# Kernel optimization log

Measured on AMD Instinct MI355X. Metric: run time of the kernel, lower is better.

Reference implementation:

```python
import jax, jax.numpy as jnp
import numpy as np

V = 1_000_000
D = 128
HS = 128
NUM_GRAPHS = 16384  # static segment count (== batch.max()+1 in the torch code)


def setup_inputs() -> dict:
    key = jax.random.key(0)
    k1, k2, k3, k4, k5 = jax.random.split(key, 5)
    H = jax.random.normal(k1, (V, D), dtype=jnp.float32)
    batch = jnp.sort(jax.random.randint(k2, (V,), 0, NUM_GRAPHS, dtype=jnp.int64))
    # nn.Linear-style init scale
    W_proj = jax.random.normal(k3, (HS, D), dtype=jnp.float32) * (1.0 / np.sqrt(D))
    b_proj = jax.random.normal(k4, (HS,), dtype=jnp.float32) * (1.0 / np.sqrt(D))
    w_score = jax.random.normal(k5, (HS,), dtype=jnp.float32) * (1.0 / np.sqrt(HS))
    return {"H": H, "batch": batch, "W_proj": W_proj, "b_proj": b_proj, "w_score": w_score}


def reference(H, batch, W_proj, b_proj, w_score):
    # e_v = a^T tanh(W h_v)            -> [V]
    e = jnp.tanh(H @ W_proj.T + b_proj) @ w_score
    # per-graph segment softmax (stable: shift by segment max)
    max_per_g = jax.ops.segment_max(e, batch, num_segments=NUM_GRAPHS)  # [G]
    a = jnp.exp(e - max_per_g[batch])
    denom = jax.ops.segment_sum(a, batch, num_segments=NUM_GRAPHS)  # [G]
    alpha = a / jnp.maximum(denom[batch], 1e-12)
    # weighted sum pooling: h_G = sum_v alpha_v h_v  -> [G, D]
    out = jax.ops.segment_sum(alpha[:, None] * H, batch, num_segments=NUM_GRAPHS)
    return out
```

## Files before the change

### kernel.cpp

```cpp
#include <hip/hip_runtime.h>
#include <hip/hip_bf16.h>
#include <hip/hip_fp16.h>

typedef __bf16 bf16x8 __attribute__((ext_vector_type(8)));
typedef float f32x4 __attribute__((ext_vector_type(4)));

constexpr int NUM_G = 16384;
constexpr int DIM = 128;
constexpr int CHUNK = 64;
constexpr int GRID1 = 768;

__global__ void seg_starts_kernel(const int* __restrict__ batch, int* __restrict__ seg, int V) {
    int v = blockIdx.x * blockDim.x + threadIdx.x;
    if (v >= V) return;
    int b1 = batch[v];
    int b0 = (v == 0) ? -1 : batch[v - 1];
    for (int g = b0 + 1; g <= b1; ++g) seg[g] = v;
    if (v == V - 1)
        for (int g = b1 + 1; g <= NUM_G; ++g) seg[g] = V;
}

__launch_bounds__(256, 3)
__global__ void attn_agg_kernel(const float* __restrict__ Hm,
                                const float* __restrict__ Wp,
                                const float* __restrict__ bp,
                                const float* __restrict__ wsc,
                                const int* __restrict__ seg,
                                float* __restrict__ out) {
    __shared__ __align__(16) __bf16 Hs[CHUNK * DIM];
    __shared__ float e_part[2][CHUNK];
    __shared__ float alpha_s[CHUNK];
    __shared__ float red[4];

    const int t = threadIdx.x;
    const int lane = t & 63;
    const int wave = t >> 6;
    const int l15 = lane & 15;
    const int lq = lane >> 4;
    const int mgrp = wave >> 1;
    const int nhalf = wave & 1;

    bf16x8 bfrag[4][4];
    float bias_n[4], wsc_n[4];
#pragma unroll
    for (int nt = 0; nt < 4; ++nt) {
        int n_g = (nhalf * 4 + nt) * 16 + l15;
        bias_n[nt] = bp[n_g];
        wsc_n[nt] = wsc[n_g];
#pragma unroll
        for (int ks = 0; ks < 4; ++ks) {
            const float* src = Wp + n_g * DIM + ks * 32 + lq * 8;
            f32x4 w0 = *(const f32x4*)src;
            f32x4 w1 = *(const f32x4*)(src + 4);
            bf16x8 f;
            f[0] = (__bf16)w0[0]; f[1] = (__bf16)w0[1]; f[2] = (__bf16)w0[2]; f[3] = (__bf16)w0[3];
            f[4] = (__bf16)w1[0]; f[5] = (__bf16)w1[1]; f[6] = (__bf16)w1[2]; f[7] = (__bf16)w1[3];
            bfrag[nt][ks] = f;
        }
    }

    for (int g = blockIdx.x; g < NUM_G; g += GRID1) {
        int v0 = seg[g];
        int n = seg[g + 1] - v0;
        float acc = 0.f;
        float lsum = 0.f;

        for (int r0 = 0; r0 < n; r0 += CHUNK) {
            int c = min(CHUNK, n - r0);
            __syncthreads();

            for (int i = t; i < c * 16; i += 256) {
                int row = i >> 4, ch = i & 15;
                const float* src = Hm + (size_t)(v0 + r0 + row) * DIM + ch * 8;
                f32x4 a0 = *(const f32x4*)src;
                f32x4 a1 = *(const f32x4*)(src + 4);
                bf16x8 hv;
                hv[0] = (__bf16)a0[0]; hv[1] = (__bf16)a0[1]; hv[2] = (__bf16)a0[2]; hv[3] = (__bf16)a0[3];
                hv[4] = (__bf16)a1[0]; hv[5] = (__bf16)a1[1]; hv[6] = (__bf16)a1[2]; hv[7] = (__bf16)a1[3];
                int chs = ch ^ (row & 15);
                *(bf16x8*)&Hs[row * DIM + chs * 8] = hv;
            }
            __syncthreads();

#pragma unroll
            for (int mt = 0; mt < 2; ++mt) {
                int mtile = mgrp * 2 + mt;
                int arow = mtile * 16 + l15;
                bf16x8 afrag[4];
#pragma unroll
                for (int ks = 0; ks < 4; ++ks) {
                    int chs = (ks * 4 + lq) ^ l15;
                    afrag[ks] = *(const bf16x8*)&Hs[arow * DIM + chs * 8];
                }
                float epl[4] = {0.f, 0.f, 0.f, 0.f};
#pragma unroll
                for (int nt = 0; nt < 4; ++nt) {
                    f32x4 dacc = {0.f, 0.f, 0.f, 0.f};
#pragma unroll
                    for (int ks = 0; ks < 4; ++ks)
                        dacc = __builtin_amdgcn_mfma_f32_16x16x32_bf16(afrag[ks], bfrag[nt][ks], dacc, 0, 0, 0);
#pragma unroll
                    for (int r = 0; r < 4; ++r) {
                        float x = dacc[r] + bias_n[nt];
                        float ex = __expf(2.f * x);
                        float th = 1.f - 2.f * __builtin_amdgcn_rcpf(ex + 1.f);
                        epl[r] += th * wsc_n[nt];
                    }
                }
#pragma unroll
                for (int m = 1; m < 16; m <<= 1)
#pragma unroll
                    for (int r = 0; r < 4; ++r)
                        epl[r] += __shfl_xor(epl[r], m, 64);
                if (l15 == 0)
#pragma unroll
                    for (int r = 0; r < 4; ++r)
                        e_part[nhalf][mtile * 16 + lq * 4 + r] = epl[r];
            }
            __syncthreads();

            float pv = 0.f;
            if (t < c) {
                float ev = e_part[0][t] + e_part[1][t];
                float p = __expf(ev);
                alpha_s[t] = p;
                pv = p;
            }
#pragma unroll
            for (int m = 1; m < 64; m <<= 1) pv += __shfl_xor(pv, m, 64);
            if (lane == 0) red[wave] = pv;
            __syncthreads();
            lsum += red[0] + red[1] + red[2] + red[3];

            if (t < 128) {
                int dch = t >> 3, doff = t & 7;
                int r = 0;
                for (; r + 4 <= c; r += 4) {
                    float p0 = alpha_s[r],     p1 = alpha_s[r + 1];
                    float p2 = alpha_s[r + 2], p3 = alpha_s[r + 3];
                    float h0 = (float)Hs[(r)     * DIM + ((dch ^ ((r)     & 15)) * 8) + doff];
                    float h1 = (float)Hs[(r + 1) * DIM + ((dch ^ ((r + 1) & 15)) * 8) + doff];
                    float h2 = (float)Hs[(r + 2) * DIM + ((dch ^ ((r + 2) & 15)) * 8) + doff];
                    float h3 = (float)Hs[(r + 3) * DIM + ((dch ^ ((r + 3) & 15)) * 8) + doff];
                    acc += p0 * h0 + p1 * h1 + p2 * h2 + p3 * h3;
                }
                for (; r < c; ++r)
                    acc += alpha_s[r] * (float)Hs[r * DIM + ((dch ^ (r & 15)) * 8) + doff];
            }
        }

        if (t < 128)
            out[(size_t)g * DIM + t] = acc / fmaxf(lsum, 1e-12f);
    }
}

extern "C" void kernel_launch(void* const* d_in, const int* in_sizes, int n_in,
                              void* d_out, int out_size, void* d_ws, size_t ws_size,
                              hipStream_t stream) {
    const float* Hm  = (const float*)d_in[0];
    const int* batch = (const int*)d_in[1];
    const float* Wp  = (const float*)d_in[2];
    const float* bp  = (const float*)d_in[3];
    const float* wsc = (const float*)d_in[4];
    float* out = (float*)d_out;
    int* seg = (int*)d_ws;
    int V = in_sizes[1];

    seg_starts_kernel<<<(V + 255) / 256, 256, 0, stream>>>(batch, seg, V);
    attn_agg_kernel<<<GRID1, 256, 0, stream>>>(Hm, Wp, bp, wsc, seg, out);
}
```

Measured before the change: 722.6 us.

## Launch one block per graph, double chunk size, split pooling across all threads

Replaces the persistent grid-stride loop over graphs with one block per graph (16384 blocks). The chunk grows from 64 to 128 rows, with MFMA tiles guarded by row count. The weighted-sum pooling now uses all 256 threads, each half taking alternate rows, and the halves are combined through shared memory at the end. The aim is better load balance and more memory parallelism. The cost is that every block reloads and converts W_proj into registers, and the larger shared-memory buffer may lower occupancy.

```diff
diff --git a/kernel.cpp b/kernel.cpp
--- a/kernel.cpp
+++ b/kernel.cpp
@@ -1,14 +1,12 @@
 #include <hip/hip_runtime.h>
 #include <hip/hip_bf16.h>
-#include <hip/hip_fp16.h>
 
 typedef __bf16 bf16x8 __attribute__((ext_vector_type(8)));
 typedef float f32x4 __attribute__((ext_vector_type(4)));
 
 constexpr int NUM_G = 16384;
 constexpr int DIM = 128;
-constexpr int CHUNK = 64;
-constexpr int GRID1 = 768;
+constexpr int CHUNK = 128;
 
 __global__ void seg_starts_kernel(const int* __restrict__ batch, int* __restrict__ seg, int V) {
     int v = blockIdx.x * blockDim.x + threadIdx.x;
@@ -30,6 +28,7 @@
     __shared__ __align__(16) __bf16 Hs[CHUNK * DIM];
     __shared__ float e_part[2][CHUNK];
     __shared__ float alpha_s[CHUNK];
+    __shared__ float wsum[2][DIM];
     __shared__ float red[4];
 
     const int t = threadIdx.x;
@@ -59,32 +58,37 @@
         }
     }
 
-    for (int g = blockIdx.x; g < NUM_G; g += GRID1) {
-        int v0 = seg[g];
-        int n = seg[g + 1] - v0;
-        float acc = 0.f;
-        float lsum = 0.f;
+    const int g = blockIdx.x;
+    const int v0 = seg[g];
+    const int n = seg[g + 1] - v0;
 
-        for (int r0 = 0; r0 < n; r0 += CHUNK) {
-            int c = min(CHUNK, n - r0);
-            __syncthreads();
+    const int col = t & 127;
+    const int hf = t >> 7;
+    const int dch = col >> 3, doff = col & 7;
+    float acc = 0.f;
+    float lsum = 0.f;
 
-            for (int i = t; i < c * 16; i += 256) {
-                int row = i >> 4, ch = i & 15;
-                const float* src = Hm + (size_t)(v0 + r0 + row) * DIM + ch * 8;
-                f32x4 a0 = *(const f32x4*)src;
-                f32x4 a1 = *(const f32x4*)(src + 4);
-                bf16x8 hv;
-                hv[0] = (__bf16)a0[0]; hv[1] = (__bf16)a0[1]; hv[2] = (__bf16)a0[2]; hv[3] = (__bf16)a0[3];
-                hv[4] = (__bf16)a1[0]; hv[5] = (__bf16)a1[1]; hv[6] = (__bf16)a1[2]; hv[7] = (__bf16)a1[3];
-                int chs = ch ^ (row & 15);
-                *(bf16x8*)&Hs[row * DIM + chs * 8] = hv;
-            }
-            __syncthreads();
+    for (int r0 = 0; r0 < n; r0 += CHUNK) {
+        int c = min(CHUNK, n - r0);
+        __syncthreads();
+
+        for (int i = t; i < c * 16; i += 256) {
+            int row = i >> 4, ch = i & 15;
+            const float* src = Hm + (size_t)(v0 + r0 + row) * DIM + ch * 8;
+            f32x4 a0 = *(const f32x4*)src;
+            f32x4 a1 = *(const f32x4*)(src + 4);
+            bf16x8 hv;
+            hv[0] = (__bf16)a0[0]; hv[1] = (__bf16)a0[1]; hv[2] = (__bf16)a0[2]; hv[3] = (__bf16)a0[3];
+            hv[4] = (__bf16)a1[0]; hv[5] = (__bf16)a1[1]; hv[6] = (__bf16)a1[2]; hv[7] = (__bf16)a1[3];
+            int chs = ch ^ (row & 15);
+            *(bf16x8*)&Hs[row * DIM + chs * 8] = hv;
+        }
+        __syncthreads();
 
 #pragma unroll
-            for (int mt = 0; mt < 2; ++mt) {
-                int mtile = mgrp * 2 + mt;
+        for (int mt = 0; mt < 4; ++mt) {
+            int mtile = mt * 2 + mgrp;
+            if (mtile * 16 < c) {
                 int arow = mtile * 16 + l15;
                 bf16x8 afrag[4];
 #pragma unroll
@@ -117,41 +121,42 @@
                     for (int r = 0; r < 4; ++r)
                         e_part[nhalf][mtile * 16 + lq * 4 + r] = epl[r];
             }
-            __syncthreads();
+        }
+        __syncthreads();
 
-            float pv = 0.f;
-            if (t < c) {
-                float ev = e_part[0][t] + e_part[1][t];
-                float p = __expf(ev);
-                alpha_s[t] = p;
-                pv = p;
+        float pv = 0.f;
+        if (t < c) {
+            float ev = e_part[0][t] + e_part[1][t];
+            float p = __expf(ev);
+            alpha_s[t] = p;
+            pv = p;
+        }
+#pragma unroll
+        for (int m = 1; m < 64; m <<= 1) pv += __shfl_xor(pv, m, 64);
+        if (lane == 0) red[wave] = pv;
+        __syncthreads();
+        lsum += red[0] + red[1] + red[2] + red[3];
+
+        {
+            int r = hf;
+            for (; r + 6 < c; r += 8) {
+                float p0 = alpha_s[r],     p1 = alpha_s[r + 2];
+                float p2 = alpha_s[r + 4], p3 = alpha_s[r + 6];
+                float h0 = (float)Hs[(r)     * DIM + ((dch ^ ((r)     & 15)) * 8) + doff];
+                float h1 = (float)Hs[(r + 2) * DIM + ((dch ^ ((r + 2) & 15)) * 8) + doff];
+                float h2 = (float)Hs[(r + 4) * DIM + ((dch ^ ((r + 4) & 15)) * 8) + doff];
+                float h3 = (float)Hs[(r + 6) * DIM + ((dch ^ ((r + 6) & 15)) * 8) + doff];
+                acc += p0 * h0 + p1 * h1 + p2 * h2 + p3 * h3;
             }
-#pragma unroll
-            for (int m = 1; m < 64; m <<= 1) pv += __shfl_xor(pv, m, 64);
-            if (lane == 0) red[wave] = pv;
-            __syncthreads();
-            lsum += red[0] + red[1] + red[2] + red[3];
+            for (; r < c; r += 2)
+                acc += alpha_s[r] * (float)Hs[r * DIM + ((dch ^ (r & 15)) * 8) + doff];
+        }
+    }
 
-            if (t < 128) {
-                int dch = t >> 3, doff = t & 7;
-                int r = 0;
-                for (; r + 4 <= c; r += 4) {
-                    float p0 = alpha_s[r],     p1 = alpha_s[r + 1];
-                    float p2 = alpha_s[r + 2], p3 = alpha_s[r + 3];
-                    float h0 = (float)Hs[(r)     * DIM + ((dch ^ ((r)     & 15)) * 8) + doff];
-                    float h1 = (float)Hs[(r + 1) * DIM + ((dch ^ ((r + 1) & 15)) * 8) + doff];
-                    float h2 = (float)Hs[(r + 2) * DIM + ((dch ^ ((r + 2) & 15)) * 8) + doff];
-                    float h3 = (float)Hs[(r + 3) * DIM + ((dch ^ ((r + 3) & 15)) * 8) + doff];
-                    acc += p0 * h0 + p1 * h1 + p2 * h2 + p3 * h3;
-                }
-                for (; r < c; ++r)
-                    acc += alpha_s[r] * (float)Hs[r * DIM + ((dch ^ (r & 15)) * 8) + doff];
-            }
-        }
-
-        if (t < 128)
-            out[(size_t)g * DIM + t] = acc / fmaxf(lsum, 1e-12f);
-    }
+    wsum[hf][col] = acc;
+    __syncthreads();
+    if (t < 128)
+        out[(size_t)g * DIM + t] = (wsum[0][t] + wsum[1][t]) / fmaxf(lsum, 1e-12f);
 }
 
 extern "C" void kernel_launch(void* const* d_in, const int* in_sizes, int n_in,
@@ -167,5 +172,5 @@
     int V = in_sizes[1];
 
     seg_starts_kernel<<<(V + 255) / 256, 256, 0, stream>>>(batch, seg, V);
-    attn_agg_kernel<<<GRID1, 256, 0, stream>>>(Hm, Wp, bp, wsc, seg, out);
+    attn_agg_kernel<<<NUM_G, 256, 0, stream>>>(Hm, Wp, bp, wsc, seg, out);
 }
```

Result: slower. 824.2 us (+14.1%).
